# Kernel tuning notes

Measured on AMD Instinct MI355X. Metric: run time of the kernel, lower is better.

Reference implementation:

```python
import jax, jax.numpy as jnp
import numpy as np

WH, WW = 7, 7          # window_size
DIM = 384
NH = 12
HD = DIM // NH
CS = 2                 # channel_scale
SCALE = HD ** -0.5
BWIN = 2048            # num_windows * batch
N = WH * WW            # kv tokens per window = 49
QN = (2 * WH) * (2 * WW)  # query tokens = 196


def _relative_position_index():
    # mirrors the torch buffer construction exactly (numpy, static)
    ch = np.repeat(np.arange(WH), 2)
    cw = np.repeat(np.arange(WW), 2)
    gh, gw = np.meshgrid(ch, cw, indexing='ij')          # (2Wh, 2Ww)
    flat = np.stack([gh.reshape(-1), gw.reshape(-1)])    # (2, 4N)
    rel = flat[:, :, None] - flat[:, None, :]            # (2, 4N, 4N)
    rel = rel[:, :, ::4]                                 # (2, 4N, N)
    rel = np.transpose(rel, (1, 2, 0)).copy()            # (4N, N, 2)
    rel[:, :, 0] += WH - 1
    rel[:, :, 1] += WW - 1
    rel[:, :, 0] *= 2 * WW - 1
    return rel.sum(-1)                                   # (4N, N) int

REL_IDX = jnp.asarray(_relative_position_index())


def setup_inputs() -> dict:
    key = jax.random.key(0)
    ks = jax.random.split(key, 9)
    tbl_rows = (2 * 2 * WH - 1) * (2 * 2 * WW - 1)       # 729
    return {
        'kv': jax.random.normal(ks[0], (BWIN, N, DIM), jnp.float32),
        'q': jax.random.normal(ks[1], (BWIN, QN, DIM // CS), jnp.float32),
        'w_kv': jax.random.normal(ks[2], (DIM, 2 * DIM), jnp.float32) * 0.02,
        'b_kv': jax.random.normal(ks[3], (2 * DIM,), jnp.float32) * 0.02,
        'w_q': jax.random.normal(ks[4], (DIM // CS, DIM), jnp.float32) * 0.02,
        'b_q': jax.random.normal(ks[5], (DIM,), jnp.float32) * 0.02,
        'bias_table': jax.random.normal(ks[6], (tbl_rows, NH), jnp.float32) * 0.02,
        'w_proj': jax.random.normal(ks[7], (DIM, DIM // CS), jnp.float32) * 0.02,
        'b_proj': jax.random.normal(ks[8], (DIM // CS,), jnp.float32) * 0.02,
    }


def reference(kv, q, w_kv, b_kv, w_q, b_q, bias_table, w_proj, b_proj):
    B, Nk, C = kv.shape
    Qn = q.shape[1]
    # projections
    kvp = kv @ w_kv + b_kv                               # (B, N, 2C)
    kvp = kvp.reshape(B, Nk, 2, NH, HD)
    k = kvp[:, :, 0]                                     # (B, N, H, hd)
    v = kvp[:, :, 1]
    qp = (q @ w_q + b_q).reshape(B, Qn, NH, HD)
    # windowed cross attention with gathered relative position bias
    attn = jnp.einsum('bqhd,bkhd->bhqk', qp * SCALE, k)  # (B, H, 4N, N)
    bias = bias_table[REL_IDX]                           # (4N, N, H)
    attn = attn + jnp.transpose(bias, (2, 0, 1))[None]
    attn = jax.nn.softmax(attn, axis=-1)
    out = jnp.einsum('bhqk,bkhd->bqhd', attn, v).reshape(B, Qn, C)
    return out @ w_proj + b_proj                          # (B, 4N, C//2)
```

## Files before the change

kernel.cpp:

```cpp
#include <hip/hip_runtime.h>

#define BWIN 2048
#define NKV  49
#define DIM  384
#define NH   12
#define HD   32
#define QN   196
#define KQ   192
#define SCALE 0.17677669529663687f

#define QS_STR  200
#define KVS_STR 392
#define KS_STR  40
#define VT_STR  72
#define P_STR   72
#define O_STR   40
#define SW_ELEMS 1792

typedef __bf16 bf16x8 __attribute__((ext_vector_type(8)));
typedef float  f32x4  __attribute__((ext_vector_type(4)));
typedef unsigned short u16;
typedef unsigned int   u32;

__device__ __forceinline__ int imin(int a, int b) { return a < b ? a : b; }

__device__ __forceinline__ u16 f2b(float f) {
    u32 u = __builtin_bit_cast(u32, f);
    return (u16)((u + 0x7fffu + ((u >> 16) & 1u)) >> 16);
}
__device__ __forceinline__ float b2f(u16 h) {
    return __builtin_bit_cast(float, ((u32)h) << 16);
}
__device__ __forceinline__ bf16x8 ld_frag(const u16* p) {
    uint4 v = *(const uint4*)p;
    return __builtin_bit_cast(bf16x8, v);
}
__device__ __forceinline__ void lds_fence() {
    asm volatile("s_waitcnt lgkmcnt(0)" ::: "memory");
}
#define MFMA(a, b, c) __builtin_amdgcn_mfma_f32_16x16x32_bf16((a), (b), (c), 0, 0, 0)

__global__ void prep_weights(const float* __restrict__ w_kv, const float* __restrict__ w_q,
                             const float* __restrict__ w_proj, u16* __restrict__ wbuf) {
    int i = blockIdx.x * 512 + threadIdx.x;
    if (i < 294912) {
        int n = i / 384, k = i % 384;
        wbuf[i] = f2b(w_kv[k * 768 + n]);
    } else if (i < 368640) {
        int j = i - 294912;
        int n = j / 192, k = j % 192;
        wbuf[i] = f2b(w_q[k * 384 + n]);
    } else {
        int j = i - 368640;
        int n = j / 384, k = j % 384;
        wbuf[i] = f2b(w_proj[k * 192 + n]);
    }
}

__global__ __launch_bounds__(512, 2) void wca_fused(
    const float* __restrict__ kv, const float* __restrict__ q,
    const float* __restrict__ b_kv, const float* __restrict__ b_q,
    const float* __restrict__ bias_table, const float* __restrict__ b_proj,
    const u16* __restrict__ wkvT, const u16* __restrict__ wqT, const u16* __restrict__ wprojT,
    float* __restrict__ out) {

    __shared__ u16 qs  [QN * QS_STR];
    __shared__ u16 kvs [NKV * KVS_STR];
    __shared__ u16 ks_s[NKV * KS_STR];
    __shared__ u16 vt_s[HD * VT_STR];
    __shared__ u16 scratch[8 * SW_ELEMS];
    __shared__ u16 bias_s[169 * 12];

    const int tid  = threadIdx.x;
    const int b    = blockIdx.x;
    const int wave = tid >> 6, lane = tid & 63, ln = lane & 15, quad = lane >> 4;

    {
        const float4* src = (const float4*)(q + (size_t)b * QN * KQ);
        for (int c = tid; c < QN * KQ / 4; c += 512) {
            int r = c / (KQ / 4), c4 = c % (KQ / 4);
            float4 f = src[c];
            ushort4 u; u.x = f2b(f.x); u.y = f2b(f.y); u.z = f2b(f.z); u.w = f2b(f.w);
            *(ushort4*)&qs[r * QS_STR + c4 * 4] = u;
        }
    }
    {
        const float4* src = (const float4*)(kv + (size_t)b * NKV * DIM);
        for (int c = tid; c < NKV * DIM / 4; c += 512) {
            int r = c / (DIM / 4), c4 = c % (DIM / 4);
            float4 f = src[c];
            ushort4 u; u.x = f2b(f.x); u.y = f2b(f.y); u.z = f2b(f.z); u.w = f2b(f.w);
            *(ushort4*)&kvs[r * KVS_STR + c4 * 4] = u;
        }
    }
    for (int c = tid; c < 169 * 12; c += 512) bias_s[c] = f2b(bias_table[c]);
    for (int c = tid; c < HD * VT_STR; c += 512) vt_s[c] = 0;
    __syncthreads();

    const int mkv = wave & 3, pkv = wave >> 2;
    const int t0 = wave, t1 = wave + 8;
    const bool has1 = (t1 < 13);

    int  kterm[4];  bool kval[4];
#pragma unroll
    for (int n = 0; n < 4; n++) {
        int kk = n * 16 + ln;
        int t4 = 4 * kk, ak = t4 / 14, bk = t4 - ak * 14;
        kterm[n] = 84 - 13 * (ak >> 1) - (bk >> 1);
        kval[n]  = (kk < NKV);
    }

    f32x4 pacc[2][12];
#pragma unroll
    for (int mi = 0; mi < 2; mi++)
#pragma unroll
        for (int nt = 0; nt < 12; nt++) pacc[mi][nt] = (f32x4){0.f, 0.f, 0.f, 0.f};

    const u16* kvs_a = &kvs[imin(mkv * 16 + ln, NKV - 1) * KVS_STR + quad * 8];
    const u16* qsa0  = &qs[imin(t0 * 16 + ln, QN - 1) * QS_STR + quad * 8];
    const u16* qsa1  = &qs[imin(t1 * 16 + ln, QN - 1) * QS_STR + quad * 8];
    u16* sw = &scratch[wave * SW_ELEMS];

    for (int h = 0; h < NH; ++h) {
        f32x4 ack = {0.f, 0.f, 0.f, 0.f}, acv = {0.f, 0.f, 0.f, 0.f};
        {
            const int ckrow = h * HD + pkv * 16 + ln;
            const u16* wk0 = &wkvT[(size_t)ckrow * 384 + quad * 8];
            const u16* wk1 = &wkvT[(size_t)(384 + ckrow) * 384 + quad * 8];
#pragma unroll
            for (int k = 0; k < 12; k++) {
                bf16x8 a = ld_frag(kvs_a + k * 32);
                ack = MFMA(a, ld_frag(wk0 + k * 32), ack);
                acv = MFMA(a, ld_frag(wk1 + k * 32), acv);
            }
        }
        {
            const int coll = pkv * 16 + ln;
            float bkb = b_kv[h * HD + coll], bvb = b_kv[384 + h * HD + coll];
#pragma unroll
            for (int r = 0; r < 4; r++) {
                int rg = mkv * 16 + quad * 4 + r;
                if (rg < NKV) {
                    ks_s[rg * KS_STR + coll] = f2b(ack[r] + bkb);
                    vt_s[coll * VT_STR + rg] = f2b(acv[r] + bvb);
                }
            }
        }
        __syncthreads();

        bf16x8 wp[12];
#pragma unroll
        for (int nt = 0; nt < 12; nt++)
            wp[nt] = ld_frag(&wprojT[(size_t)(nt * 16 + ln) * 384 + h * HD + quad * 8]);

        f32x4 qa[2][2];
#pragma unroll
        for (int mi = 0; mi < 2; mi++)
#pragma unroll
            for (int n = 0; n < 2; n++) qa[mi][n] = (f32x4){0.f, 0.f, 0.f, 0.f};
        {
            const u16* wq0 = &wqT[(size_t)(h * HD + ln) * KQ + quad * 8];
            const u16* wq1 = &wqT[(size_t)(h * HD + 16 + ln) * KQ + quad * 8];
#pragma unroll
            for (int k = 0; k < 6; k++) {
                bf16x8 b0 = ld_frag(wq0 + k * 32);
                bf16x8 b1 = ld_frag(wq1 + k * 32);
                bf16x8 a0 = ld_frag(qsa0 + k * 32);
                qa[0][0] = MFMA(a0, b0, qa[0][0]);
                qa[0][1] = MFMA(a0, b1, qa[0][1]);
                if (has1) {
                    bf16x8 a1 = ld_frag(qsa1 + k * 32);
                    qa[1][0] = MFMA(a1, b0, qa[1][0]);
                    qa[1][1] = MFMA(a1, b1, qa[1][1]);
                }
            }
        }
        {
            float bq0 = b_q[h * HD + ln], bq1 = b_q[h * HD + 16 + ln];
#pragma unroll
            for (int mi = 0; mi < 2; mi++) {
                if (mi && !has1) break;
#pragma unroll
                for (int r = 0; r < 4; r++) {
                    sw[mi * 640 + (quad * 4 + r) * O_STR + ln]      = f2b((qa[mi][0][r] + bq0) * SCALE);
                    sw[mi * 640 + (quad * 4 + r) * O_STR + 16 + ln] = f2b((qa[mi][1][r] + bq1) * SCALE);
                }
            }
        }
        lds_fence();

#pragma unroll
        for (int mi2 = 0; mi2 < 2; mi2++) {
            int mi = 1 - mi2;
            if (mi == 1 && !has1) continue;
            int t = mi ? t1 : t0;

            bf16x8 aq = ld_frag(&sw[mi * 640 + ln * O_STR + quad * 8]);
            f32x4 s[4];
#pragma unroll
            for (int n = 0; n < 4; n++) {
                bf16x8 bk = ld_frag(&ks_s[imin(n * 16 + ln, NKV - 1) * KS_STR + quad * 8]);
                f32x4 z = {0.f, 0.f, 0.f, 0.f};
                s[n] = MFMA(aq, bk, z);
            }
            float rsum[4];
#pragma unroll
            for (int r = 0; r < 4; r++) {
                int qrow = t * 16 + quad * 4 + r;
                int qb = imin(qrow, QN - 1);
                int aqd = qb / 14, bqd = qb - aqd * 14;
                int qterm = 13 * (aqd >> 1) + (bqd >> 1);
                float sv[4];
#pragma unroll
                for (int n = 0; n < 4; n++) {
                    if (kval[n]) sv[n] = s[n][r] + b2f(bias_s[(qterm + kterm[n]) * 12 + h]);
                    else         sv[n] = -1e30f;
                }
                float mx = fmaxf(fmaxf(sv[0], sv[1]), fmaxf(sv[2], sv[3]));
                mx = fmaxf(mx, __shfl_xor(mx, 1));
                mx = fmaxf(mx, __shfl_xor(mx, 2));
                mx = fmaxf(mx, __shfl_xor(mx, 4));
                mx = fmaxf(mx, __shfl_xor(mx, 8));
                float e[4], sum = 0.f;
#pragma unroll
                for (int n = 0; n < 4; n++) { e[n] = __expf(sv[n] - mx); sum += e[n]; }
                sum += __shfl_xor(sum, 1);
                sum += __shfl_xor(sum, 2);
                sum += __shfl_xor(sum, 4);
                sum += __shfl_xor(sum, 8);
                rsum[r] = sum;
#pragma unroll
                for (int n = 0; n < 4; n++)
                    sw[640 + (quad * 4 + r) * P_STR + n * 16 + ln] = f2b(e[n]);
            }
            lds_fence();

            bf16x8 ap0 = ld_frag(&sw[640 + ln * P_STR + quad * 8]);
            bf16x8 ap1 = ld_frag(&sw[640 + ln * P_STR + 32 + quad * 8]);
            bf16x8 bv00 = ld_frag(&vt_s[ln * VT_STR + quad * 8]);
            bf16x8 bv01 = ld_frag(&vt_s[ln * VT_STR + 32 + quad * 8]);
            bf16x8 bv10 = ld_frag(&vt_s[(16 + ln) * VT_STR + quad * 8]);
            bf16x8 bv11 = ld_frag(&vt_s[(16 + ln) * VT_STR + 32 + quad * 8]);
            f32x4 o0 = {0.f, 0.f, 0.f, 0.f}, o1 = {0.f, 0.f, 0.f, 0.f};
            o0 = MFMA(ap0, bv00, o0); o0 = MFMA(ap1, bv01, o0);
            o1 = MFMA(ap0, bv10, o1); o1 = MFMA(ap1, bv11, o1);
            lds_fence();
#pragma unroll
            for (int r = 0; r < 4; r++) {
                float rinv = 1.0f / rsum[r];
                sw[1152 + (quad * 4 + r) * O_STR + ln]      = f2b(o0[r] * rinv);
                sw[1152 + (quad * 4 + r) * O_STR + 16 + ln] = f2b(o1[r] * rinv);
            }
            lds_fence();

            bf16x8 ao = ld_frag(&sw[1152 + ln * O_STR + quad * 8]);
#pragma unroll
            for (int nt = 0; nt < 12; nt++) pacc[mi][nt] = MFMA(ao, wp[nt], pacc[mi][nt]);
        }
        __syncthreads();
    }

#pragma unroll
    for (int mi = 0; mi < 2; mi++) {
        if (mi && !has1) break;
        int t = mi ? t1 : t0;
#pragma unroll
        for (int r = 0; r < 4; r++) {
            int qrow = t * 16 + quad * 4 + r;
            if (qrow < QN) {
                float* orow = out + ((size_t)b * QN + qrow) * KQ;
#pragma unroll
                for (int nt = 0; nt < 12; nt++)
                    orow[nt * 16 + ln] = pacc[mi][nt][r] + b_proj[nt * 16 + ln];
            }
        }
    }
}

extern "C" void kernel_launch(void* const* d_in, const int* in_sizes, int n_in,
                              void* d_out, int out_size, void* d_ws, size_t ws_size,
                              hipStream_t stream) {
    (void)in_sizes; (void)n_in; (void)out_size; (void)ws_size;
    const float* kv         = (const float*)d_in[0];
    const float* q          = (const float*)d_in[1];
    const float* w_kv       = (const float*)d_in[2];
    const float* b_kv       = (const float*)d_in[3];
    const float* w_q        = (const float*)d_in[4];
    const float* b_q        = (const float*)d_in[5];
    const float* bias_table = (const float*)d_in[6];
    const float* w_proj     = (const float*)d_in[7];
    const float* b_proj     = (const float*)d_in[8];
    float* out = (float*)d_out;
    u16* wbuf = (u16*)d_ws;

    prep_weights<<<864, 512, 0, stream>>>(w_kv, w_q, w_proj, wbuf);
    wca_fused<<<BWIN, 512, 0, stream>>>(kv, q, b_kv, b_q, bias_table, b_proj,
                                        wbuf, wbuf + 294912, wbuf + 368640, out);
}
```

Measured before the change: 2.130 ms.

## Assign one wave per head and stream query tiles through fused attention

Reorganizes the fused kernel from 8 waves looping over heads to 12 waves, one per head. All K/V projections are computed once up front, and query rows are streamed in 16-row tiles, each tile fully projected, attended and output-projected before the next. This removes the per-head barrier loop and the full-window q staging buffer in LDS, and keeps Wq fragments in registers. The cost is one block barrier pair per query tile (13 tiles), with the output projection reading all heads' outputs from shared memory. Occupancy also changes to 768 threads per block with a different LDS footprint.

Result: faster. 1.732 ms (-18.7%).

```diff
diff --git a/kernel.cpp b/kernel.cpp
--- a/kernel.cpp
+++ b/kernel.cpp
@@ -9,13 +9,22 @@
 #define KQ   192
 #define SCALE 0.17677669529663687f
 
-#define QS_STR  200
-#define KVS_STR 392
-#define KS_STR  40
+#define KS_STR  392
 #define VT_STR  72
+#define QT_STR  200
+#define OB_STR  40
+#define QP_STR  40
 #define P_STR   72
-#define O_STR   40
-#define SW_ELEMS 1792
+
+#define OFF_KS   0
+#define OFF_VT   (NKV * KS_STR)
+#define OFF_BIAS (OFF_VT + NH * HD * VT_STR)
+#define OFF_UC   (OFF_BIAS + 169 * NH)
+#define OFF_QT   OFF_UC
+#define OFF_OB   (OFF_QT + 16 * QT_STR)
+#define OFF_QP   (OFF_OB + NH * 16 * OB_STR)
+#define OFF_P    (OFF_QP + NH * 16 * QP_STR)
+#define LDS_TOT  (OFF_P + NH * 16 * P_STR)
 
 typedef __bf16 bf16x8 __attribute__((ext_vector_type(8)));
 typedef float  f32x4  __attribute__((ext_vector_type(4)));
@@ -57,223 +66,221 @@
     }
 }
 
-__global__ __launch_bounds__(512, 2) void wca_fused(
+__global__ __launch_bounds__(768, 3) void wca_fused(
     const float* __restrict__ kv, const float* __restrict__ q,
     const float* __restrict__ b_kv, const float* __restrict__ b_q,
     const float* __restrict__ bias_table, const float* __restrict__ b_proj,
     const u16* __restrict__ wkvT, const u16* __restrict__ wqT, const u16* __restrict__ wprojT,
     float* __restrict__ out) {
 
-    __shared__ u16 qs  [QN * QS_STR];
-    __shared__ u16 kvs [NKV * KVS_STR];
-    __shared__ u16 ks_s[NKV * KS_STR];
-    __shared__ u16 vt_s[HD * VT_STR];
-    __shared__ u16 scratch[8 * SW_ELEMS];
-    __shared__ u16 bias_s[169 * 12];
+    __shared__ u16 lds[LDS_TOT];
 
     const int tid  = threadIdx.x;
     const int b    = blockIdx.x;
     const int wave = tid >> 6, lane = tid & 63, ln = lane & 15, quad = lane >> 4;
-
-    {
-        const float4* src = (const float4*)(q + (size_t)b * QN * KQ);
-        for (int c = tid; c < QN * KQ / 4; c += 512) {
-            int r = c / (KQ / 4), c4 = c % (KQ / 4);
-            float4 f = src[c];
-            ushort4 u; u.x = f2b(f.x); u.y = f2b(f.y); u.z = f2b(f.z); u.w = f2b(f.w);
-            *(ushort4*)&qs[r * QS_STR + c4 * 4] = u;
-        }
-    }
+    const int h    = wave;
+
+    u16* ks     = lds + OFF_KS;
+    u16* vt     = lds + OFF_VT;
+    u16* bias_s = lds + OFF_BIAS;
+    u16* kvs    = lds + OFF_UC;
+    u16* qtile  = lds + OFF_QT;
+    u16* obuf   = lds + OFF_OB;
+    u16* qp_s   = lds + OFF_QP + h * (16 * QP_STR);
+    u16* P_s    = lds + OFF_P  + h * (16 * P_STR);
+
     {
         const float4* src = (const float4*)(kv + (size_t)b * NKV * DIM);
-        for (int c = tid; c < NKV * DIM / 4; c += 512) {
+        for (int c = tid; c < NKV * DIM / 4; c += 768) {
             int r = c / (DIM / 4), c4 = c % (DIM / 4);
             float4 f = src[c];
             ushort4 u; u.x = f2b(f.x); u.y = f2b(f.y); u.z = f2b(f.z); u.w = f2b(f.w);
-            *(ushort4*)&kvs[r * KVS_STR + c4 * 4] = u;
-        }
-    }
-    for (int c = tid; c < 169 * 12; c += 512) bias_s[c] = f2b(bias_table[c]);
-    for (int c = tid; c < HD * VT_STR; c += 512) vt_s[c] = 0;
+            *(ushort4*)&kvs[r * KS_STR + c4 * 4] = u;
+        }
+        for (int c = tid; c < 169 * NH; c += 768) bias_s[c] = f2b(bias_table[c]);
+        for (int c = tid; c < NH * HD * VT_STR; c += 768) vt[c] = 0;
+    }
     __syncthreads();
 
-    const int mkv = wave & 3, pkv = wave >> 2;
-    const int t0 = wave, t1 = wave + 8;
-    const bool has1 = (t1 < 13);
+    {
+        const int cb = h * HD;
+        f32x4 acc[4][4];
+#pragma unroll
+        for (int j = 0; j < 4; j++)
+#pragma unroll
+            for (int m = 0; m < 4; m++) acc[j][m] = (f32x4){0.f, 0.f, 0.f, 0.f};
+        const u16* wb[4] = {
+            wkvT + (size_t)(cb + ln) * DIM,
+            wkvT + (size_t)(cb + 16 + ln) * DIM,
+            wkvT + (size_t)(DIM + cb + ln) * DIM,
+            wkvT + (size_t)(DIM + cb + 16 + ln) * DIM };
+        const u16* ar[4] = {
+            &kvs[imin(ln,      NKV - 1) * KS_STR],
+            &kvs[imin(16 + ln, NKV - 1) * KS_STR],
+            &kvs[imin(32 + ln, NKV - 1) * KS_STR],
+            &kvs[imin(48 + ln, NKV - 1) * KS_STR] };
+#pragma unroll
+        for (int k = 0; k < 12; k++) {
+            bf16x8 b0 = ld_frag(wb[0] + k * 32 + quad * 8);
+            bf16x8 b1 = ld_frag(wb[1] + k * 32 + quad * 8);
+            bf16x8 b2 = ld_frag(wb[2] + k * 32 + quad * 8);
+            bf16x8 b3 = ld_frag(wb[3] + k * 32 + quad * 8);
+#pragma unroll
+            for (int m = 0; m < 4; m++) {
+                bf16x8 a = ld_frag(ar[m] + k * 32 + quad * 8);
+                acc[0][m] = MFMA(a, b0, acc[0][m]);
+                acc[1][m] = MFMA(a, b1, acc[1][m]);
+                acc[2][m] = MFMA(a, b2, acc[2][m]);
+                acc[3][m] = MFMA(a, b3, acc[3][m]);
+            }
+        }
+        float bk0 = b_kv[cb + ln],       bk1 = b_kv[cb + 16 + ln];
+        float bv0 = b_kv[DIM + cb + ln], bv1 = b_kv[DIM + cb + 16 + ln];
+        u16* vth = vt + h * (HD * VT_STR);
+#pragma unroll
+        for (int m = 0; m < 4; m++)
+#pragma unroll
+            for (int r = 0; r < 4; r++) {
+                int kk = m * 16 + quad * 4 + r;
+                if (kk < NKV) {
+                    ks[kk * KS_STR + cb + ln]      = f2b(acc[0][m][r] + bk0);
+                    ks[kk * KS_STR + cb + 16 + ln] = f2b(acc[1][m][r] + bk1);
+                    vth[ln * VT_STR + kk]          = f2b(acc[2][m][r] + bv0);
+                    vth[(16 + ln) * VT_STR + kk]   = f2b(acc[3][m][r] + bv1);
+                }
+            }
+    }
+    __syncthreads();
 
     int  kterm[4];  bool kval[4];
 #pragma unroll
     for (int n = 0; n < 4; n++) {
         int kk = n * 16 + ln;
-        int t4 = 4 * kk, ak = t4 / 14, bk = t4 - ak * 14;
-        kterm[n] = 84 - 13 * (ak >> 1) - (bk >> 1);
+        int t4 = 4 * kk, kA = t4 / 14, kB = t4 - kA * 14;
+        kterm[n] = 84 - 13 * (kA >> 1) - (kB >> 1);
         kval[n]  = (kk < NKV);
     }
-
-    f32x4 pacc[2][12];
-#pragma unroll
-    for (int mi = 0; mi < 2; mi++)
-#pragma unroll
-        for (int nt = 0; nt < 12; nt++) pacc[mi][nt] = (f32x4){0.f, 0.f, 0.f, 0.f};
-
-    const u16* kvs_a = &kvs[imin(mkv * 16 + ln, NKV - 1) * KVS_STR + quad * 8];
-    const u16* qsa0  = &qs[imin(t0 * 16 + ln, QN - 1) * QS_STR + quad * 8];
-    const u16* qsa1  = &qs[imin(t1 * 16 + ln, QN - 1) * QS_STR + quad * 8];
-    u16* sw = &scratch[wave * SW_ELEMS];
-
-    for (int h = 0; h < NH; ++h) {
-        f32x4 ack = {0.f, 0.f, 0.f, 0.f}, acv = {0.f, 0.f, 0.f, 0.f};
+    const float bq0 = b_q[h * HD + ln], bq1 = b_q[h * HD + 16 + ln];
+    const float bpj = b_proj[h * 16 + ln];
+    const f32x4 z4 = {0.f, 0.f, 0.f, 0.f};
+
+    bf16x8 wqf[2][6];
+#pragma unroll
+    for (int k = 0; k < 6; k++) {
+        wqf[0][k] = ld_frag(&wqT[(size_t)(h * HD + ln) * KQ + k * 32 + quad * 8]);
+        wqf[1][k] = ld_frag(&wqT[(size_t)(h * HD + 16 + ln) * KQ + k * 32 + quad * 8]);
+    }
+
+    {
+        int rr = tid / 48, c4 = tid % 48;
+        int qrow = imin(rr, QN - 1);
+        float4 f = *(const float4*)(q + ((size_t)b * QN + qrow) * KQ + c4 * 4);
+        ushort4 u; u.x = f2b(f.x); u.y = f2b(f.y); u.z = f2b(f.z); u.w = f2b(f.w);
+        *(ushort4*)&qtile[rr * QT_STR + c4 * 4] = u;
+    }
+    __syncthreads();
+
+    for (int t = 0; t < 13; ++t) {
+        f32x4 qa0 = z4, qa1 = z4;
         {
-            const int ckrow = h * HD + pkv * 16 + ln;
-            const u16* wk0 = &wkvT[(size_t)ckrow * 384 + quad * 8];
-            const u16* wk1 = &wkvT[(size_t)(384 + ckrow) * 384 + quad * 8];
-#pragma unroll
-            for (int k = 0; k < 12; k++) {
-                bf16x8 a = ld_frag(kvs_a + k * 32);
-                ack = MFMA(a, ld_frag(wk0 + k * 32), ack);
-                acv = MFMA(a, ld_frag(wk1 + k * 32), acv);
-            }
-        }
+            const u16* qrp = &qtile[ln * QT_STR + quad * 8];
+#pragma unroll
+            for (int k = 0; k < 6; k++) {
+                bf16x8 a = ld_frag(qrp + k * 32);
+                qa0 = MFMA(a, wqf[0][k], qa0);
+                qa1 = MFMA(a, wqf[1][k], qa1);
+            }
+        }
+#pragma unroll
+        for (int r = 0; r < 4; r++) {
+            qp_s[(quad * 4 + r) * QP_STR + ln]      = f2b((qa0[r] + bq0) * SCALE);
+            qp_s[(quad * 4 + r) * QP_STR + 16 + ln] = f2b((qa1[r] + bq1) * SCALE);
+        }
+        lds_fence();
+
+        bf16x8 aq = ld_frag(&qp_s[ln * QP_STR + quad * 8]);
+        f32x4 s[4];
+#pragma unroll
+        for (int n = 0; n < 4; n++) {
+            bf16x8 bk = ld_frag(&ks[imin(n * 16 + ln, NKV - 1) * KS_STR + h * HD + quad * 8]);
+            s[n] = MFMA(aq, bk, z4);
+        }
+        float rsum[4];
+#pragma unroll
+        for (int r = 0; r < 4; r++) {
+            int qrow = t * 16 + quad * 4 + r;
+            int qb = imin(qrow, QN - 1);
+            int aqd = qb / 14, bqd = qb - aqd * 14;
+            int qterm = 13 * (aqd >> 1) + (bqd >> 1);
+            float sv[4];
+#pragma unroll
+            for (int n = 0; n < 4; n++) {
+                if (kval[n]) sv[n] = s[n][r] + b2f(bias_s[(qterm + kterm[n]) * NH + h]);
+                else         sv[n] = -1e30f;
+            }
+            float mx = fmaxf(fmaxf(sv[0], sv[1]), fmaxf(sv[2], sv[3]));
+            mx = fmaxf(mx, __shfl_xor(mx, 1));
+            mx = fmaxf(mx, __shfl_xor(mx, 2));
+            mx = fmaxf(mx, __shfl_xor(mx, 4));
+            mx = fmaxf(mx, __shfl_xor(mx, 8));
+            float e[4], sum = 0.f;
+#pragma unroll
+            for (int n = 0; n < 4; n++) { e[n] = __expf(sv[n] - mx); sum += e[n]; }
+            sum += __shfl_xor(sum, 1);
+            sum += __shfl_xor(sum, 2);
+            sum += __shfl_xor(sum, 4);
+            sum += __shfl_xor(sum, 8);
+            rsum[r] = sum;
+#pragma unroll
+            for (int n = 0; n < 4; n++)
+                P_s[(quad * 4 + r) * P_STR + n * 16 + ln] = f2b(e[n]);
+        }
+        lds_fence();
+
         {
-            const int coll = pkv * 16 + ln;
-            float bkb = b_kv[h * HD + coll], bvb = b_kv[384 + h * HD + coll];
+            bf16x8 ap0 = ld_frag(&P_s[ln * P_STR + quad * 8]);
+            bf16x8 ap1 = ld_frag(&P_s[ln * P_STR + 32 + quad * 8]);
+            const u16* vth = &vt[h * (HD * VT_STR)];
+            bf16x8 bv00 = ld_frag(&vth[ln * VT_STR + quad * 8]);
+            bf16x8 bv01 = ld_frag(&vth[ln * VT_STR + 32 + quad * 8]);
+            bf16x8 bv10 = ld_frag(&vth[(16 + ln) * VT_STR + quad * 8]);
+            bf16x8 bv11 = ld_frag(&vth[(16 + ln) * VT_STR + 32 + quad * 8]);
+            f32x4 o0 = MFMA(ap0, bv00, z4); o0 = MFMA(ap1, bv01, o0);
+            f32x4 o1 = MFMA(ap0, bv10, z4); o1 = MFMA(ap1, bv11, o1);
 #pragma unroll
             for (int r = 0; r < 4; r++) {
-                int rg = mkv * 16 + quad * 4 + r;
-                if (rg < NKV) {
-                    ks_s[rg * KS_STR + coll] = f2b(ack[r] + bkb);
-                    vt_s[coll * VT_STR + rg] = f2b(acv[r] + bvb);
-                }
+                float rinv = 1.0f / rsum[r];
+                obuf[h * 640 + (quad * 4 + r) * OB_STR + ln]      = f2b(o0[r] * rinv);
+                obuf[h * 640 + (quad * 4 + r) * OB_STR + 16 + ln] = f2b(o1[r] * rinv);
             }
         }
         __syncthreads();
 
-        bf16x8 wp[12];
-#pragma unroll
-        for (int nt = 0; nt < 12; nt++)
-            wp[nt] = ld_frag(&wprojT[(size_t)(nt * 16 + ln) * 384 + h * HD + quad * 8]);
-
-        f32x4 qa[2][2];
-#pragma unroll
-        for (int mi = 0; mi < 2; mi++)
-#pragma unroll
-            for (int n = 0; n < 2; n++) qa[mi][n] = (f32x4){0.f, 0.f, 0.f, 0.f};
+        if (t < 12) {
+            int rr = tid / 48, c4 = tid % 48;
+            int qrow = imin((t + 1) * 16 + rr, QN - 1);
+            float4 f = *(const float4*)(q + ((size_t)b * QN + qrow) * KQ + c4 * 4);
+            ushort4 u; u.x = f2b(f.x); u.y = f2b(f.y); u.z = f2b(f.z); u.w = f2b(f.w);
+            *(ushort4*)&qtile[rr * QT_STR + c4 * 4] = u;
+        }
+
         {
-            const u16* wq0 = &wqT[(size_t)(h * HD + ln) * KQ + quad * 8];
-            const u16* wq1 = &wqT[(size_t)(h * HD + 16 + ln) * KQ + quad * 8];
-#pragma unroll
-            for (int k = 0; k < 6; k++) {
-                bf16x8 b0 = ld_frag(wq0 + k * 32);
-                bf16x8 b1 = ld_frag(wq1 + k * 32);
-                bf16x8 a0 = ld_frag(qsa0 + k * 32);
-                qa[0][0] = MFMA(a0, b0, qa[0][0]);
-                qa[0][1] = MFMA(a0, b1, qa[0][1]);
-                if (has1) {
-                    bf16x8 a1 = ld_frag(qsa1 + k * 32);
-                    qa[1][0] = MFMA(a1, b0, qa[1][0]);
-                    qa[1][1] = MFMA(a1, b1, qa[1][1]);
-                }
-            }
-        }
-        {
-            float bq0 = b_q[h * HD + ln], bq1 = b_q[h * HD + 16 + ln];
-#pragma unroll
-            for (int mi = 0; mi < 2; mi++) {
-                if (mi && !has1) break;
-#pragma unroll
-                for (int r = 0; r < 4; r++) {
-                    sw[mi * 640 + (quad * 4 + r) * O_STR + ln]      = f2b((qa[mi][0][r] + bq0) * SCALE);
-                    sw[mi * 640 + (quad * 4 + r) * O_STR + 16 + ln] = f2b((qa[mi][1][r] + bq1) * SCALE);
-                }
-            }
-        }
-        lds_fence();
-
-#pragma unroll
-        for (int mi2 = 0; mi2 < 2; mi2++) {
-            int mi = 1 - mi2;
-            if (mi == 1 && !has1) continue;
-            int t = mi ? t1 : t0;
-
-            bf16x8 aq = ld_frag(&sw[mi * 640 + ln * O_STR + quad * 8]);
-            f32x4 s[4];
-#pragma unroll
-            for (int n = 0; n < 4; n++) {
-                bf16x8 bk = ld_frag(&ks_s[imin(n * 16 + ln, NKV - 1) * KS_STR + quad * 8]);
-                f32x4 z = {0.f, 0.f, 0.f, 0.f};
-                s[n] = MFMA(aq, bk, z);
-            }
-            float rsum[4];
+            f32x4 p0 = z4, p1 = z4;
+#pragma unroll
+            for (int hh = 0; hh < NH; hh += 2) {
+                p0 = MFMA(ld_frag(&obuf[hh * 640 + ln * OB_STR + quad * 8]),
+                          ld_frag(&wprojT[(size_t)(h * 16 + ln) * DIM + hh * HD + quad * 8]), p0);
+                p1 = MFMA(ld_frag(&obuf[(hh + 1) * 640 + ln * OB_STR + quad * 8]),
+                          ld_frag(&wprojT[(size_t)(h * 16 + ln) * DIM + (hh + 1) * HD + quad * 8]), p1);
+            }
 #pragma unroll
             for (int r = 0; r < 4; r++) {
                 int qrow = t * 16 + quad * 4 + r;
-                int qb = imin(qrow, QN - 1);
-                int aqd = qb / 14, bqd = qb - aqd * 14;
-                int qterm = 13 * (aqd >> 1) + (bqd >> 1);
-                float sv[4];
-#pragma unroll
-                for (int n = 0; n < 4; n++) {
-                    if (kval[n]) sv[n] = s[n][r] + b2f(bias_s[(qterm + kterm[n]) * 12 + h]);
-                    else         sv[n] = -1e30f;
-                }
-                float mx = fmaxf(fmaxf(sv[0], sv[1]), fmaxf(sv[2], sv[3]));
-                mx = fmaxf(mx, __shfl_xor(mx, 1));
-                mx = fmaxf(mx, __shfl_xor(mx, 2));
-                mx = fmaxf(mx, __shfl_xor(mx, 4));
-                mx = fmaxf(mx, __shfl_xor(mx, 8));
-                float e[4], sum = 0.f;
-#pragma unroll
-                for (int n = 0; n < 4; n++) { e[n] = __expf(sv[n] - mx); sum += e[n]; }
-                sum += __shfl_xor(sum, 1);
-                sum += __shfl_xor(sum, 2);
-                sum += __shfl_xor(sum, 4);
-                sum += __shfl_xor(sum, 8);
-                rsum[r] = sum;
-#pragma unroll
-                for (int n = 0; n < 4; n++)
-                    sw[640 + (quad * 4 + r) * P_STR + n * 16 + ln] = f2b(e[n]);
-            }
-            lds_fence();
-
-            bf16x8 ap0 = ld_frag(&sw[640 + ln * P_STR + quad * 8]);
-            bf16x8 ap1 = ld_frag(&sw[640 + ln * P_STR + 32 + quad * 8]);
-            bf16x8 bv00 = ld_frag(&vt_s[ln * VT_STR + quad * 8]);
-            bf16x8 bv01 = ld_frag(&vt_s[ln * VT_STR + 32 + quad * 8]);
-            bf16x8 bv10 = ld_frag(&vt_s[(16 + ln) * VT_STR + quad * 8]);
-            bf16x8 bv11 = ld_frag(&vt_s[(16 + ln) * VT_STR + 32 + quad * 8]);
-            f32x4 o0 = {0.f, 0.f, 0.f, 0.f}, o1 = {0.f, 0.f, 0.f, 0.f};
-            o0 = MFMA(ap0, bv00, o0); o0 = MFMA(ap1, bv01, o0);
-            o1 = MFMA(ap0, bv10, o1); o1 = MFMA(ap1, bv11, o1);
-            lds_fence();
-#pragma unroll
-            for (int r = 0; r < 4; r++) {
-                float rinv = 1.0f / rsum[r];
-                sw[1152 + (quad * 4 + r) * O_STR + ln]      = f2b(o0[r] * rinv);
-                sw[1152 + (quad * 4 + r) * O_STR + 16 + ln] = f2b(o1[r] * rinv);
-            }
-            lds_fence();
-
-            bf16x8 ao = ld_frag(&sw[1152 + ln * O_STR + quad * 8]);
-#pragma unroll
-            for (int nt = 0; nt < 12; nt++) pacc[mi][nt] = MFMA(ao, wp[nt], pacc[mi][nt]);
+                if (qrow < QN)
+                    out[((size_t)b * QN + qrow) * KQ + h * 16 + ln] = p0[r] + p1[r] + bpj;
+            }
         }
         __syncthreads();
-    }
-
-#pragma unroll
-    for (int mi = 0; mi < 2; mi++) {
-        if (mi && !has1) break;
-        int t = mi ? t1 : t0;
-#pragma unroll
-        for (int r = 0; r < 4; r++) {
-            int qrow = t * 16 + quad * 4 + r;
-            if (qrow < QN) {
-                float* orow = out + ((size_t)b * QN + qrow) * KQ;
-#pragma unroll
-                for (int nt = 0; nt < 12; nt++)
-                    orow[nt * 16 + ln] = pacc[mi][nt][r] + b_proj[nt * 16 + ln];
-            }
-        }
     }
 }
 
@@ -294,6 +301,6 @@
     u16* wbuf = (u16*)d_ws;
 
     prep_weights<<<864, 512, 0, stream>>>(w_kv, w_q, w_proj, wbuf);
-    wca_fused<<<BWIN, 512, 0, stream>>>(kv, q, b_kv, b_q, bias_table, b_proj,
+    wca_fused<<<BWIN, 768, 0, stream>>>(kv, q, b_kv, b_q, bias_table, b_proj,
                                         wbuf, wbuf + 294912, wbuf + 368640, out);
 }
```
